# Optimization experiments

Measured on AMD Instinct MI355X. Metric: run time of the kernel, lower is better.

The kernel has to match this reference:

```python
import jax, jax.numpy as jnp
import numpy as np

EMB_DIM = 300
VOCAB_X = 50000
VOCAB_Y = 50000
LEN_X = 64
LEN_Y = 64
BATCH = 1024
PAD_ID = 0


def setup_inputs() -> dict:
    key = jax.random.key(0)
    k1, k2, k3, k4, k5, k6, k7 = jax.random.split(key, 7)
    initrange = 0.5 / EMB_DIM
    emb_x = jax.random.uniform(k1, (VOCAB_X, EMB_DIM), jnp.float32, -initrange, initrange)
    emb_y = jax.random.uniform(k2, (VOCAB_Y, EMB_DIM), jnp.float32, -initrange, initrange)
    # padding row zeroed as in init_emb
    emb_x = emb_x.at[PAD_ID].set(0.0)
    emb_y = emb_y.at[PAD_ID].set(0.0)
    return {
        "samp_hid": jax.random.normal(k3, (BATCH, EMB_DIM), jnp.float32),
        "batch_x": jax.random.randint(k4, (BATCH, LEN_X), 0, VOCAB_X, jnp.int64 if jax.config.jax_enable_x64 else jnp.int32),
        "batch_y": jax.random.randint(k5, (BATCH, LEN_Y), 0, VOCAB_Y, jnp.int64 if jax.config.jax_enable_x64 else jnp.int32),
        "emb_x": emb_x,
        "emb_y": emb_y,
        "bias_x": jax.random.uniform(k6, (VOCAB_X,), jnp.float32),
        "bias_y": jax.random.uniform(k7, (VOCAB_Y,), jnp.float32),
    }


def _cal_nll(z, tokens, emb, bias):
    # logits shared across all positions: [B, V]
    logits = z @ emb.T + bias
    logp = jax.nn.log_softmax(logits, axis=-1)            # compute log-softmax ONCE per row
    tok_logp = jnp.take_along_axis(logp, tokens, axis=1)  # [B, L] gather per-position targets
    mask = (tokens != PAD_ID).astype(logits.dtype)        # CrossEntropyLoss(ignore_index=0)
    return jnp.sum(-tok_logp * mask, axis=1)              # sum over positions -> [B]


def reference(samp_hid, batch_x, batch_y, emb_x, emb_y, bias_x, bias_y):
    nll_x = _cal_nll(samp_hid, batch_x, emb_x, bias_x)
    nll_y = _cal_nll(samp_hid, batch_y, emb_y, bias_y)
    return jnp.mean(nll_x + nll_y)
```

## Files before the change

### kernel.cpp

```cpp
#include <hip/hip_runtime.h>

#define V_VOCAB 50000
#define K_DIM   300
#define NROWS   1024
#define LEN     64
#define NBC     392
#define NCG     1568
#define KS      19
#define PASSES  32
#define LOG2E   1.44269504088896f

typedef __attribute__((ext_vector_type(8)))  short bf16x8;
typedef __attribute__((ext_vector_type(16))) float f32x16;

static __device__ __forceinline__ unsigned short f2bf(float f) {
    unsigned int u = __builtin_bit_cast(unsigned int, f);
    u = u + 0x7fffu + ((u >> 16) & 1u);
    return (unsigned short)(u >> 16);
}

static __device__ __forceinline__ f32x16 zero16() {
    f32x16 z;
#pragma unroll
    for (int i = 0; i < 16; ++i) z[i] = 0.0f;
    return z;
}

static __device__ __forceinline__ void gload_lds16(const void* g, void* l) {
    __builtin_amdgcn_global_load_lds((const __attribute__((address_space(1))) void*)g,
                                     (__attribute__((address_space(3))) void*)l, 16, 0, 0);
}

__global__ void zbf_kernel(const float* __restrict__ z, unsigned short* __restrict__ zbf) {
    int t = blockIdx.x * 256 + threadIdx.x;
    int l    = t & 63;
    int rest = t >> 6;
    int ks   = rest % KS;
    int rblk = rest / KS;
    int row  = rblk * 32 + (l & 31);
    int k0   = ks * 16 + (l >> 5) * 8;
    unsigned short o[8];
#pragma unroll
    for (int j = 0; j < 8; ++j) {
        int k = k0 + j;
        float v = (k < K_DIM) ? z[row * K_DIM + k] * LOG2E
                              : ((k == K_DIM) ? LOG2E : 0.0f);
        o[j] = f2bf(v);
    }
    ushort4* p = (ushort4*)(zbf + (size_t)t * 8);
    p[0] = make_ushort4(o[0], o[1], o[2], o[3]);
    p[1] = make_ushort4(o[4], o[5], o[6], o[7]);
}

__global__ void __launch_bounds__(256, 2)
gemm_kernel(const unsigned short* __restrict__ zbf,
            const float* __restrict__ emb_x,
            const float* __restrict__ emb_y,
            const float* __restrict__ bias_x,
            const float* __restrict__ bias_y,
            float* __restrict__ partial,
            float* __restrict__ lsesum,
            int accmode) {
    __shared__ unsigned short Zs[2][9728];

    const int tid  = threadIdx.x;
    const int lane = tid & 63;
    const int w    = tid >> 6;
    const int side = blockIdx.y;
    const int bc   = blockIdx.x;
    const float* eg = side ? emb_y : emb_x;
    const float* bg = side ? bias_y : bias_x;

    {
        const unsigned short* src = zbf;
#pragma unroll
        for (int i = 0; i < 5; ++i) {
            int q = w * 5 + i;
            if (q > 18) q = 18;
            gload_lds16(src + (size_t)q * 512 + lane * 8, &Zs[0][q * 512]);
        }
    }

    bf16x8 a[KS];
    {
        const int c  = bc * 128 + w * 32 + (lane & 31);
        const bool cv = (c < V_VOCAB);
        const float* erow = eg + (size_t)c * K_DIM;
        const int khi = (lane >> 5) * 8;
#pragma unroll
        for (int ks = 0; ks < KS; ++ks) {
            const int k0 = ks * 16 + khi;
            float f[8];
            if (k0 + 8 <= K_DIM) {
                float4 u  = cv ? *(const float4*)(erow + k0)     : make_float4(0, 0, 0, 0);
                float4 v2 = cv ? *(const float4*)(erow + k0 + 4) : make_float4(0, 0, 0, 0);
                f[0] = u.x;  f[1] = u.y;  f[2] = u.z;  f[3] = u.w;
                f[4] = v2.x; f[5] = v2.y; f[6] = v2.z; f[7] = v2.w;
            } else {
#pragma unroll
                for (int j = 0; j < 8; ++j) {
                    int k = k0 + j;
                    f[j] = (k < K_DIM) ? (cv ? erow[k] : 0.0f)
                         : (k == K_DIM ? (cv ? bg[c] : -3e38f) : 0.0f);
                }
            }
            bf16x8 t;
#pragma unroll
            for (int j = 0; j < 8; ++j) t[j] = (short)f2bf(f[j]);
            a[ks] = t;
        }
    }

    float* pout = partial + ((size_t)side * NCG + (size_t)bc * 4 + w) * NROWS;
    float* lout = lsesum + side * NROWS;

    int buf = 0;
    for (int p = 0; p < PASSES; ++p) {
        if (p < PASSES - 1) {
            const unsigned short* src = zbf + (size_t)(p + 1) * 9728;
#pragma unroll
            for (int i = 0; i < 5; ++i) {
                int q = w * 5 + i;
                if (q > 18) q = 18;
                gload_lds16(src + (size_t)q * 512 + lane * 8, &Zs[buf ^ 1][q * 512]);
            }
            asm volatile("s_waitcnt vmcnt(5)" ::: "memory");
        } else {
            asm volatile("s_waitcnt vmcnt(0)" ::: "memory");
        }
        __builtin_amdgcn_s_barrier();
        __builtin_amdgcn_sched_barrier(0);

        const unsigned short* zb = &Zs[buf][0];
        f32x16 accE = zero16(), accO = zero16();
#pragma unroll
        for (int ks = 0; ks < KS; ks += 2) {
            bf16x8 b0 = *(const bf16x8*)(zb + ((size_t)ks * 64 + lane) * 8);
            accE = __builtin_amdgcn_mfma_f32_32x32x16_bf16(a[ks], b0, accE, 0, 0, 0);
            if (ks + 1 < KS) {
                bf16x8 b1 = *(const bf16x8*)(zb + ((size_t)(ks + 1) * 64 + lane) * 8);
                accO = __builtin_amdgcn_mfma_f32_32x32x16_bf16(a[ks + 1], b1, accO, 0, 0, 0);
            }
        }

        float s = 0.0f;
#pragma unroll
        for (int r = 0; r < 16; ++r) s += exp2f(accE[r] + accO[r]);
        s += __shfl_xor(s, 32, 64);
        if (accmode) { if (lane < 32) atomicAdd(lout + p * 32 + lane, s); }
        else         { if (lane < 32) pout[p * 32 + lane] = s; }

        __builtin_amdgcn_s_barrier();
        buf ^= 1;
    }
}

__global__ void lse_kernel(const float* __restrict__ partial, float* __restrict__ lse) {
    __shared__ float red[1024];
    int side = blockIdx.x >> 4;
    int mg   = blockIdx.x & 15;
    int m    = mg * 64 + (threadIdx.x & 63);
    int sg   = threadIdx.x >> 6;
    const float* p = partial + (size_t)side * NCG * NROWS;
    float s = 0.0f;
    for (int cg = sg; cg < NCG; cg += 16)
        s += p[(size_t)cg * NROWS + m];
    red[threadIdx.x] = s;
    __syncthreads();
    if (threadIdx.x < 64) {
        float t = 0.0f;
#pragma unroll
        for (int j = 0; j < 16; ++j) t += red[threadIdx.x + 64 * j];
        lse[side * NROWS + mg * 64 + threadIdx.x] = logf(t);
    }
}

__global__ void lse_log_kernel(float* __restrict__ lsesum) {
    int g = blockIdx.x * 1024 + threadIdx.x;
    if (g < 2 * NROWS) lsesum[g] = logf(lsesum[g]);
}

__global__ void gatherdot_kernel(const float* __restrict__ z,
                                 const int* __restrict__ tok_x, const int* __restrict__ tok_y,
                                 const float* __restrict__ emb_x, const float* __restrict__ emb_y,
                                 const float* __restrict__ bias_x, const float* __restrict__ bias_y,
                                 const float* __restrict__ lse, float* __restrict__ gdpart) {
    __shared__ float gs[304];
    const int b = blockIdx.x, side = blockIdx.y & 1, half = blockIdx.y >> 1;
    const int tid = threadIdx.x;
    const int* tokp = (side ? tok_y : tok_x) + b * LEN + half * 32;
    const float* eg = side ? emb_y : emb_x;
    if (tid < K_DIM) {
        float g0 = 0.0f, g1 = 0.0f, g2 = 0.0f, g3 = 0.0f;
#pragma unroll 4
        for (int pos = 0; pos < 32; pos += 4) {
            int t0 = tokp[pos], t1 = tokp[pos + 1], t2 = tokp[pos + 2], t3 = tokp[pos + 3];
            if (t0) g0 += eg[(size_t)t0 * K_DIM + tid];
            if (t1) g1 += eg[(size_t)t1 * K_DIM + tid];
            if (t2) g2 += eg[(size_t)t2 * K_DIM + tid];
            if (t3) g3 += eg[(size_t)t3 * K_DIM + tid];
        }
        gs[tid] = (g0 + g1) + (g2 + g3);
    }
    __syncthreads();
    if (tid < 64) {
        const float* bg = side ? bias_y : bias_x;
        float dp = 0.0f;
#pragma unroll
        for (int i = 0; i < 5; ++i) {
            int d = tid + i * 64;
            if (d < K_DIM) dp += z[(size_t)b * K_DIM + d] * gs[d];
        }
        int t = (tid < 32) ? tokp[tid] : 0;
        float bs = t ? bg[t] : 0.0f;
        float ct = t ? 1.0f : 0.0f;
#pragma unroll
        for (int off = 32; off > 0; off >>= 1) {
            dp += __shfl_xor(dp, off, 64);
            bs += __shfl_xor(bs, off, 64);
            ct += __shfl_xor(ct, off, 64);
        }
        if (tid == 0)
            gdpart[((size_t)side * NROWS + b) * 2 + half] =
                ct * lse[side * NROWS + b] - dp - bs;
    }
}

__global__ void finalize_kernel(const float* __restrict__ gdpart, float* __restrict__ out) {
    __shared__ float r16[16];
    int i = threadIdx.x;
    float v = gdpart[i * 2] + gdpart[i * 2 + 1]
            + gdpart[(NROWS + i) * 2] + gdpart[(NROWS + i) * 2 + 1];
#pragma unroll
    for (int off = 32; off > 0; off >>= 1) v += __shfl_xor(v, off, 64);
    if ((i & 63) == 0) r16[i >> 6] = v;
    __syncthreads();
    if (i < 64) {
        float x = (i < 16) ? r16[i] : 0.0f;
#pragma unroll
        for (int off = 8; off > 0; off >>= 1) x += __shfl_xor(x, off, 64);
        if (i == 0) out[0] = x * (1.0f / 1024.0f);
    }
}

extern "C" void kernel_launch(void* const* d_in, const int* in_sizes, int n_in,
                              void* d_out, int out_size, void* d_ws, size_t ws_size,
                              hipStream_t stream) {
    const float* z      = (const float*)d_in[0];
    const int*   tok_x  = (const int*)d_in[1];
    const int*   tok_y  = (const int*)d_in[2];
    const float* emb_x  = (const float*)d_in[3];
    const float* emb_y  = (const float*)d_in[4];
    const float* bias_x = (const float*)d_in[5];
    const float* bias_y = (const float*)d_in[6];
    float* out = (float*)d_out;

    char* ws = (char*)d_ws;
    const size_t ZBF_B  = 622592;
    const size_t PART_B = (size_t)2 * NCG * NROWS * 4;
    const size_t need   = ZBF_B + PART_B + 8192 + 16384;

    unsigned short* zbf = (unsigned short*)ws;
    zbf_kernel<<<152, 256, 0, stream>>>(z, zbf);

    if (ws_size >= need) {
        float* partial = (float*)(ws + ZBF_B);
        float* lse     = (float*)(ws + ZBF_B + PART_B);
        float* gdpart  = (float*)(ws + ZBF_B + PART_B + 8192);
        gemm_kernel<<<dim3(NBC, 2), 256, 0, stream>>>(zbf, emb_x, emb_y, bias_x, bias_y,
                                                      partial, lse , 0);
        lse_kernel<<<32, 1024, 0, stream>>>(partial, lse);
        gatherdot_kernel<<<dim3(NROWS, 4), 320, 0, stream>>>(z, tok_x, tok_y, emb_x, emb_y,
                                                             bias_x, bias_y, lse, gdpart);
        finalize_kernel<<<1, 1024, 0, stream>>>(gdpart, out);
    } else {
        float* lse    = (float*)(ws + ZBF_B);
        float* gdpart = (float*)(ws + ZBF_B + 8192);
        hipMemsetAsync(lse, 0, 8192, stream);
        gemm_kernel<<<dim3(NBC, 2), 256, 0, stream>>>(zbf, emb_x, emb_y, bias_x, bias_y,
                                                      gdpart , lse, 1);
        lse_log_kernel<<<2, 1024, 0, stream>>>(lse);
        gatherdot_kernel<<<dim3(NROWS, 4), 320, 0, stream>>>(z, tok_x, tok_y, emb_x, emb_y,
                                                             bias_x, bias_y, lse, gdpart);
        finalize_kernel<<<1, 1024, 0, stream>>>(gdpart, out);
    }
}
```

Measured before the change: 182.2 us.

## Process 64 rows per pass with doubled LDS tile and hardware exp

Each pass now loads two 32-row Z tiles into a doubled LDS buffer, so the number of passes is halved. Every register-resident embedding fragment feeds four independent MFMA accumulator chains instead of two, which gives more independent matrix work per loaded tile. The exp2f call is replaced by inline v_exp_f32, and the prefetch wait moves to the end of each pass, leaving one barrier per pass instead of two. In exchange, LDS use doubles and accumulator registers grow, which may reduce occupancy under launch_bounds(256,2). The raw hardware exp also skips the denormal handling that exp2f provides.

```diff
diff --git a/kernel.cpp b/kernel.cpp
--- a/kernel.cpp
+++ b/kernel.cpp
@@ -7,7 +7,7 @@
 #define NBC     392
 #define NCG     1568
 #define KS      19
-#define PASSES  32
+#define PASSES  16
 #define LOG2E   1.44269504088896f
 
 typedef __attribute__((ext_vector_type(8)))  short bf16x8;
@@ -24,6 +24,12 @@
 #pragma unroll
     for (int i = 0; i < 16; ++i) z[i] = 0.0f;
     return z;
+}
+
+static __device__ __forceinline__ float exp2_hw(float x) {
+    float r;
+    asm volatile("v_exp_f32 %0, %1" : "=v"(r) : "v"(x));
+    return r;
 }
 
 static __device__ __forceinline__ void gload_lds16(const void* g, void* l) {
@@ -61,7 +67,7 @@
             float* __restrict__ partial,
             float* __restrict__ lsesum,
             int accmode) {
-    __shared__ unsigned short Zs[2][9728];
+    __shared__ unsigned short Zs[2][19456];
 
     const int tid  = threadIdx.x;
     const int lane = tid & 63;
@@ -74,9 +80,9 @@
     {
         const unsigned short* src = zbf;
 #pragma unroll
-        for (int i = 0; i < 5; ++i) {
-            int q = w * 5 + i;
-            if (q > 18) q = 18;
+        for (int i = 0; i < 10; ++i) {
+            int q = w * 10 + i;
+            if (q >= 38) q -= 8;
             gload_lds16(src + (size_t)q * 512 + lane * 8, &Zs[0][q * 512]);
         }
     }
@@ -114,42 +120,50 @@
     float* pout = partial + ((size_t)side * NCG + (size_t)bc * 4 + w) * NROWS;
     float* lout = lsesum + side * NROWS;
 
+    asm volatile("s_waitcnt vmcnt(0)" ::: "memory");
+    __builtin_amdgcn_s_barrier();
+
     int buf = 0;
     for (int p = 0; p < PASSES; ++p) {
         if (p < PASSES - 1) {
-            const unsigned short* src = zbf + (size_t)(p + 1) * 9728;
-#pragma unroll
-            for (int i = 0; i < 5; ++i) {
-                int q = w * 5 + i;
-                if (q > 18) q = 18;
+            const unsigned short* src = zbf + (size_t)(p + 1) * 19456;
+#pragma unroll
+            for (int i = 0; i < 10; ++i) {
+                int q = w * 10 + i;
+                if (q >= 38) q -= 8;
                 gload_lds16(src + (size_t)q * 512 + lane * 8, &Zs[buf ^ 1][q * 512]);
             }
-            asm volatile("s_waitcnt vmcnt(5)" ::: "memory");
-        } else {
-            asm volatile("s_waitcnt vmcnt(0)" ::: "memory");
-        }
-        __builtin_amdgcn_s_barrier();
-        __builtin_amdgcn_sched_barrier(0);
+        }
 
         const unsigned short* zb = &Zs[buf][0];
-        f32x16 accE = zero16(), accO = zero16();
+        f32x16 a0e = zero16(), a0o = zero16(), a1e = zero16(), a1o = zero16();
 #pragma unroll
         for (int ks = 0; ks < KS; ks += 2) {
             bf16x8 b0 = *(const bf16x8*)(zb + ((size_t)ks * 64 + lane) * 8);
-            accE = __builtin_amdgcn_mfma_f32_32x32x16_bf16(a[ks], b0, accE, 0, 0, 0);
+            a0e = __builtin_amdgcn_mfma_f32_32x32x16_bf16(a[ks], b0, a0e, 0, 0, 0);
+            bf16x8 b1 = *(const bf16x8*)(zb + ((size_t)(KS + ks) * 64 + lane) * 8);
+            a1e = __builtin_amdgcn_mfma_f32_32x32x16_bf16(a[ks], b1, a1e, 0, 0, 0);
             if (ks + 1 < KS) {
-                bf16x8 b1 = *(const bf16x8*)(zb + ((size_t)(ks + 1) * 64 + lane) * 8);
-                accO = __builtin_amdgcn_mfma_f32_32x32x16_bf16(a[ks + 1], b1, accO, 0, 0, 0);
+                bf16x8 c0 = *(const bf16x8*)(zb + ((size_t)(ks + 1) * 64 + lane) * 8);
+                a0o = __builtin_amdgcn_mfma_f32_32x32x16_bf16(a[ks + 1], c0, a0o, 0, 0, 0);
+                bf16x8 c1 = *(const bf16x8*)(zb + ((size_t)(KS + ks + 1) * 64 + lane) * 8);
+                a1o = __builtin_amdgcn_mfma_f32_32x32x16_bf16(a[ks + 1], c1, a1o, 0, 0, 0);
             }
         }
 
-        float s = 0.0f;
-#pragma unroll
-        for (int r = 0; r < 16; ++r) s += exp2f(accE[r] + accO[r]);
-        s += __shfl_xor(s, 32, 64);
-        if (accmode) { if (lane < 32) atomicAdd(lout + p * 32 + lane, s); }
-        else         { if (lane < 32) pout[p * 32 + lane] = s; }
-
+        float s0 = 0.0f, s1 = 0.0f;
+#pragma unroll
+        for (int r = 0; r < 16; ++r) {
+            s0 += exp2_hw(a0e[r] + a0o[r]);
+            s1 += exp2_hw(a1e[r] + a1o[r]);
+        }
+        s0 += __shfl_xor(s0, 32, 64);
+        s1 += __shfl_xor(s1, 32, 64);
+        float val = (lane < 32) ? s0 : s1;
+        if (accmode) { if (lane < 64) atomicAdd(lout + p * 64 + lane, val); }
+        else         { pout[p * 64 + lane] = val; }
+
+        asm volatile("s_waitcnt vmcnt(0)" ::: "memory");
         __builtin_amdgcn_s_barrier();
         buf ^= 1;
     }
```

Result: faster. 169.1 us (-7.2%).

## Use 1024-thread GEMM blocks sharing larger Z tiles, split gather-dot into quarters

Applied to the files above, without the earlier changes.

The GEMM kernel now runs 16 waves per block and covers 512 vocab columns per block. That cuts the grid from 392 to 98 column blocks, so each staged Z tile in LDS is reused by four times as many waves. Each pass stages 128 rows, four 32-row sub-blocks, into a double buffer of about 155 KB. The wait for the prefetch is moved after compute, and the per-pass barrier count drops. exp2f is replaced with raw v_exp_f32. The gather-dot kernel is split into four token quarters instead of two, giving more blocks. Risks: the LDS footprint nearly fills the CU, a single block per CU may leave less latency hiding, and the vmcnt(5) wait now comes after the stores, which may not guarantee the prefetch has landed.

```diff
diff --git a/kernel.cpp b/kernel.cpp
--- a/kernel.cpp
+++ b/kernel.cpp
@@ -4,10 +4,10 @@
 #define K_DIM   300
 #define NROWS   1024
 #define LEN     64
-#define NBC     392
+#define NBC     98
 #define NCG     1568
 #define KS      19
-#define PASSES  32
+#define PASSES  8
 #define LOG2E   1.44269504088896f
 
 typedef __attribute__((ext_vector_type(8)))  short bf16x8;
@@ -24,6 +24,12 @@
 #pragma unroll
     for (int i = 0; i < 16; ++i) z[i] = 0.0f;
     return z;
+}
+
+static __device__ __forceinline__ float exp2_hw(float x) {
+    float r;
+    asm volatile("v_exp_f32 %0, %1" : "=v"(r) : "v"(x));
+    return r;
 }
 
 static __device__ __forceinline__ void gload_lds16(const void* g, void* l) {
@@ -52,7 +58,7 @@
     p[1] = make_ushort4(o[4], o[5], o[6], o[7]);
 }
 
-__global__ void __launch_bounds__(256, 2)
+__global__ void __launch_bounds__(1024)
 gemm_kernel(const unsigned short* __restrict__ zbf,
             const float* __restrict__ emb_x,
             const float* __restrict__ emb_y,
@@ -61,7 +67,7 @@
             float* __restrict__ partial,
             float* __restrict__ lsesum,
             int accmode) {
-    __shared__ unsigned short Zs[2][9728];
+    __shared__ unsigned short Zs[2][38912];
 
     const int tid  = threadIdx.x;
     const int lane = tid & 63;
@@ -76,14 +82,14 @@
 #pragma unroll
         for (int i = 0; i < 5; ++i) {
             int q = w * 5 + i;
-            if (q > 18) q = 18;
+            if (q > 75) q = 75;
             gload_lds16(src + (size_t)q * 512 + lane * 8, &Zs[0][q * 512]);
         }
     }
 
     bf16x8 a[KS];
     {
-        const int c  = bc * 128 + w * 32 + (lane & 31);
+        const int c  = bc * 512 + w * 32 + (lane & 31);
         const bool cv = (c < V_VOCAB);
         const float* erow = eg + (size_t)c * K_DIM;
         const int khi = (lane >> 5) * 8;
@@ -111,45 +117,50 @@
         }
     }
 
-    float* pout = partial + ((size_t)side * NCG + (size_t)bc * 4 + w) * NROWS;
+    float* pout = partial + ((size_t)side * NCG + (size_t)bc * 16 + w) * NROWS;
     float* lout = lsesum + side * NROWS;
+
+    asm volatile("s_waitcnt vmcnt(0)" ::: "memory");
+    __builtin_amdgcn_s_barrier();
 
     int buf = 0;
     for (int p = 0; p < PASSES; ++p) {
         if (p < PASSES - 1) {
-            const unsigned short* src = zbf + (size_t)(p + 1) * 9728;
+            const unsigned short* src = zbf + (size_t)(p + 1) * 38912;
 #pragma unroll
             for (int i = 0; i < 5; ++i) {
                 int q = w * 5 + i;
-                if (q > 18) q = 18;
+                if (q > 75) q = 75;
                 gload_lds16(src + (size_t)q * 512 + lane * 8, &Zs[buf ^ 1][q * 512]);
             }
+        }
+
+#pragma unroll 1
+        for (int rb = 0; rb < 4; ++rb) {
+            const unsigned short* zb = &Zs[buf][rb * 9728];
+            f32x16 accE = zero16(), accO = zero16();
+#pragma unroll
+            for (int ks = 0; ks < KS; ks += 2) {
+                bf16x8 b0 = *(const bf16x8*)(zb + ((size_t)ks * 64 + lane) * 8);
+                accE = __builtin_amdgcn_mfma_f32_32x32x16_bf16(a[ks], b0, accE, 0, 0, 0);
+                if (ks + 1 < KS) {
+                    bf16x8 b1 = *(const bf16x8*)(zb + ((size_t)(ks + 1) * 64 + lane) * 8);
+                    accO = __builtin_amdgcn_mfma_f32_32x32x16_bf16(a[ks + 1], b1, accO, 0, 0, 0);
+                }
+            }
+            float s = 0.0f;
+#pragma unroll
+            for (int r = 0; r < 16; ++r) s += exp2_hw(accE[r] + accO[r]);
+            s += __shfl_xor(s, 32, 64);
+            if (accmode) { if (lane < 32) atomicAdd(lout + p * 128 + rb * 32 + lane, s); }
+            else         { if (lane < 32) pout[p * 128 + rb * 32 + lane] = s; }
+        }
+
+        if (p < PASSES - 1) {
             asm volatile("s_waitcnt vmcnt(5)" ::: "memory");
         } else {
             asm volatile("s_waitcnt vmcnt(0)" ::: "memory");
         }
-        __builtin_amdgcn_s_barrier();
-        __builtin_amdgcn_sched_barrier(0);
-
-        const unsigned short* zb = &Zs[buf][0];
-        f32x16 accE = zero16(), accO = zero16();
-#pragma unroll
-        for (int ks = 0; ks < KS; ks += 2) {
-            bf16x8 b0 = *(const bf16x8*)(zb + ((size_t)ks * 64 + lane) * 8);
-            accE = __builtin_amdgcn_mfma_f32_32x32x16_bf16(a[ks], b0, accE, 0, 0, 0);
-            if (ks + 1 < KS) {
-                bf16x8 b1 = *(const bf16x8*)(zb + ((size_t)(ks + 1) * 64 + lane) * 8);
-                accO = __builtin_amdgcn_mfma_f32_32x32x16_bf16(a[ks + 1], b1, accO, 0, 0, 0);
-            }
-        }
-
-        float s = 0.0f;
-#pragma unroll
-        for (int r = 0; r < 16; ++r) s += exp2f(accE[r] + accO[r]);
-        s += __shfl_xor(s, 32, 64);
-        if (accmode) { if (lane < 32) atomicAdd(lout + p * 32 + lane, s); }
-        else         { if (lane < 32) pout[p * 32 + lane] = s; }
-
         __builtin_amdgcn_s_barrier();
         buf ^= 1;
     }
@@ -186,14 +197,14 @@
                                  const float* __restrict__ bias_x, const float* __restrict__ bias_y,
                                  const float* __restrict__ lse, float* __restrict__ gdpart) {
     __shared__ float gs[304];
-    const int b = blockIdx.x, side = blockIdx.y & 1, half = blockIdx.y >> 1;
+    const int b = blockIdx.x, side = blockIdx.y & 1, quarter = blockIdx.y >> 1;
     const int tid = threadIdx.x;
-    const int* tokp = (side ? tok_y : tok_x) + b * LEN + half * 32;
+    const int* tokp = (side ? tok_y : tok_x) + b * LEN + quarter * 16;
     const float* eg = side ? emb_y : emb_x;
     if (tid < K_DIM) {
         float g0 = 0.0f, g1 = 0.0f, g2 = 0.0f, g3 = 0.0f;
 #pragma unroll 4
-        for (int pos = 0; pos < 32; pos += 4) {
+        for (int pos = 0; pos < 16; pos += 4) {
             int t0 = tokp[pos], t1 = tokp[pos + 1], t2 = tokp[pos + 2], t3 = tokp[pos + 3];
             if (t0) g0 += eg[(size_t)t0 * K_DIM + tid];
             if (t1) g1 += eg[(size_t)t1 * K_DIM + tid];
@@ -211,7 +222,7 @@
             int d = tid + i * 64;
             if (d < K_DIM) dp += z[(size_t)b * K_DIM + d] * gs[d];
         }
-        int t = (tid < 32) ? tokp[tid] : 0;
+        int t = (tid < 16) ? tokp[tid] : 0;
         float bs = t ? bg[t] : 0.0f;
         float ct = t ? 1.0f : 0.0f;
 #pragma unroll
@@ -221,7 +232,7 @@
             ct += __shfl_xor(ct, off, 64);
         }
         if (tid == 0)
-            gdpart[((size_t)side * NROWS + b) * 2 + half] =
+            gdpart[((size_t)side * NROWS + b) * 4 + quarter] =
                 ct * lse[side * NROWS + b] - dp - bs;
     }
 }
@@ -229,8 +240,10 @@
 __global__ void finalize_kernel(const float* __restrict__ gdpart, float* __restrict__ out) {
     __shared__ float r16[16];
     int i = threadIdx.x;
-    float v = gdpart[i * 2] + gdpart[i * 2 + 1]
-            + gdpart[(NROWS + i) * 2] + gdpart[(NROWS + i) * 2 + 1];
+    float v = 0.0f;
+#pragma unroll
+    for (int q = 0; q < 4; ++q)
+        v += gdpart[(size_t)i * 4 + q] + gdpart[((size_t)NROWS + i) * 4 + q];
 #pragma unroll
     for (int off = 32; off > 0; off >>= 1) v += __shfl_xor(v, off, 64);
     if ((i & 63) == 0) r16[i >> 6] = v;
@@ -258,7 +271,7 @@
     char* ws = (char*)d_ws;
     const size_t ZBF_B  = 622592;
     const size_t PART_B = (size_t)2 * NCG * NROWS * 4;
-    const size_t need   = ZBF_B + PART_B + 8192 + 16384;
+    const size_t need   = ZBF_B + PART_B + 8192 + 32768;
 
     unsigned short* zbf = (unsigned short*)ws;
     zbf_kernel<<<152, 256, 0, stream>>>(z, zbf);
@@ -267,20 +280,20 @@
         float* partial = (float*)(ws + ZBF_B);
         float* lse     = (float*)(ws + ZBF_B + PART_B);
         float* gdpart  = (float*)(ws + ZBF_B + PART_B + 8192);
-        gemm_kernel<<<dim3(NBC, 2), 256, 0, stream>>>(zbf, emb_x, emb_y, bias_x, bias_y,
-                                                      partial, lse , 0);
+        gemm_kernel<<<dim3(NBC, 2), 1024, 0, stream>>>(zbf, emb_x, emb_y, bias_x, bias_y,
+                                                       partial, lse , 0);
         lse_kernel<<<32, 1024, 0, stream>>>(partial, lse);
-        gatherdot_kernel<<<dim3(NROWS, 4), 320, 0, stream>>>(z, tok_x, tok_y, emb_x, emb_y,
+        gatherdot_kernel<<<dim3(NROWS, 8), 320, 0, stream>>>(z, tok_x, tok_y, emb_x, emb_y,
                                                              bias_x, bias_y, lse, gdpart);
         finalize_kernel<<<1, 1024, 0, stream>>>(gdpart, out);
     } else {
         float* lse    = (float*)(ws + ZBF_B);
         float* gdpart = (float*)(ws + ZBF_B + 8192);
         hipMemsetAsync(lse, 0, 8192, stream);
-        gemm_kernel<<<dim3(NBC, 2), 256, 0, stream>>>(zbf, emb_x, emb_y, bias_x, bias_y,
-                                                      gdpart , lse, 1);
+        gemm_kernel<<<dim3(NBC, 2), 1024, 0, stream>>>(zbf, emb_x, emb_y, bias_x, bias_y,
+                                                       gdpart , lse, 1);
         lse_log_kernel<<<2, 1024, 0, stream>>>(lse);
-        gatherdot_kernel<<<dim3(NROWS, 4), 320, 0, stream>>>(z, tok_x, tok_y, emb_x, emb_y,
+        gatherdot_kernel<<<dim3(NROWS, 8), 320, 0, stream>>>(z, tok_x, tok_y, emb_x, emb_y,
                                                              bias_x, bias_y, lse, gdpart);
         finalize_kernel<<<1, 1024, 0, stream>>>(gdpart, out);
     }
```

Measured after the change: 189.8 us. 4.2% more time.
